# Kernel optimization log

Measured on AMD Instinct MI355X. Metric: run time of the kernel, lower is better.

The kernel has to match this reference:

```python
import jax, jax.numpy as jnp
import numpy as np
import math

N_EMBED = 1024
N_HEAD = 16
HS = N_EMBED // N_HEAD

def setup_inputs() -> dict:
    key = jax.random.key(0)
    ks = jax.random.split(key, 5)
    s = 1.0 / math.sqrt(N_EMBED)
    x = jax.random.normal(ks[0], (2, 2048, N_EMBED), dtype=jnp.float32)
    W_qkv = jax.random.uniform(ks[1], (N_EMBED, 3 * N_EMBED), dtype=jnp.float32, minval=-s, maxval=s)
    b_qkv = jax.random.uniform(ks[2], (3 * N_EMBED,), dtype=jnp.float32, minval=-s, maxval=s)
    W_out = jax.random.uniform(ks[3], (N_EMBED, N_EMBED), dtype=jnp.float32, minval=-s, maxval=s)
    b_out = jax.random.uniform(ks[4], (N_EMBED,), dtype=jnp.float32, minval=-s, maxval=s)
    return {"x": x, "W_qkv": W_qkv, "b_qkv": b_qkv, "W_out": W_out, "b_out": b_out}

def reference(x, W_qkv, b_qkv, W_out, b_out):
    bs, seq_len, dim = x.shape
    qkv = x @ W_qkv + b_qkv                      # [b, s, 3*d]
    q, k, v = jnp.split(qkv, 3, axis=-1)
    def heads(t):
        return t.reshape(bs, seq_len, N_HEAD, HS).transpose(0, 2, 1, 3)  # [b, h, s, hs]
    q, k, v = heads(q), heads(k), heads(v)
    scale = 1.0 / math.sqrt(HS)
    attn = jnp.einsum('bhqd,bhkd->bhqk', q, k) * scale  # [b, h, s, s]
    causal = jnp.tril(jnp.ones((seq_len, seq_len), dtype=bool))
    attn = jnp.where(causal, attn, -jnp.inf)
    attn = jax.nn.softmax(attn, axis=-1)
    o = jnp.einsum('bhqk,bhkd->bhqd', attn, v)   # [b, h, s, hs]
    o = o.transpose(0, 2, 1, 3).reshape(bs, seq_len, dim)
    return o @ W_out + b_out
```

## Files before the change

### kernel.cpp

```cpp
#include <hip/hip_runtime.h>
#include <hip/hip_bf16.h>
#include <stdint.h>

typedef __attribute__((ext_vector_type(4))) float f32x4;
typedef __attribute__((ext_vector_type(8))) short s16x8;
typedef __attribute__((ext_vector_type(4))) short s16x4;

#define B_   2
#define S_   2048
#define D_   1024
#define H_   16
#define HS_  64
#define TOK  (B_*S_)
#define BH_  (B_*H_)

__device__ __forceinline__ short f2bf(float f){
  union { float f; uint32_t u; } v; v.f = f;
  uint32_t u = v.u;
  u += 0x7fffu + ((u >> 16) & 1u);
  return (short)(u >> 16);
}

__device__ __forceinline__ uint32_t cvt_pk_bf16(float lo, float hi){
  uint32_t r;
  asm("v_cvt_pk_bf16_f32 %0, %1, %2" : "=v"(r) : "v"(lo), "v"(hi));
  return r;
}

__device__ __forceinline__ void gload_lds16(const void* g, void* l){
  __builtin_amdgcn_global_load_lds((const __attribute__((address_space(1))) void*)g,
                                   (__attribute__((address_space(3))) void*)l, 16, 0, 0);
}

__global__ void k_cvt(const float* __restrict__ src, short* __restrict__ dst, int n4){
  int i = blockIdx.x * blockDim.x + threadIdx.x;
  if (i < n4){
    float4 v = reinterpret_cast<const float4*>(src)[i];
    s16x4 o;
    o.x = f2bf(v.x); o.y = f2bf(v.y); o.z = f2bf(v.z); o.w = f2bf(v.w);
    reinterpret_cast<s16x4*>(dst)[i] = o;
  }
}

__global__ void k_tconv(const float* __restrict__ src, short* __restrict__ dst, int K, int N){
  __shared__ short tile[32][33];
  const int n0 = blockIdx.x * 32, k0 = blockIdx.y * 32;
  const int c = threadIdx.x & 31, r8 = threadIdx.x >> 5;
  #pragma unroll
  for (int j = 0; j < 4; j++){
    int k = r8 + j * 8;
    tile[c][k] = f2bf(src[(size_t)(k0 + k) * N + n0 + c]);
  }
  __syncthreads();
  #pragma unroll
  for (int j = 0; j < 4; j++){
    int nl = r8 + j * 8;
    dst[(size_t)(n0 + nl) * K + k0 + c] = tile[nl][c];
  }
}

template<int EPI>
__global__ __launch_bounds__(256, 2) void k_gemm(
    const short* __restrict__ A, const short* __restrict__ Bt,
    const float* __restrict__ bias, void* __restrict__ outp)
{
  __shared__ short Al[128 * 32];
  __shared__ short Bl[128 * 32];
  const int tid = threadIdx.x;
  const int lane = tid & 63, wave = tid >> 6;
  const int m0 = blockIdx.x * 128, n0 = blockIdx.y * 128;
  const int wm = (wave >> 1) * 64, wn = (wave & 1) * 64;
  const int c = lane & 15, g = lane >> 4;

  f32x4 acc[4][4];
  #pragma unroll
  for (int i = 0; i < 4; i++)
    #pragma unroll
    for (int j = 0; j < 4; j++) acc[i][j] = (f32x4){0.f, 0.f, 0.f, 0.f};

  const short* Asrc = A + (size_t)m0 * 1024;
  const short* Bsrc = Bt + (size_t)n0 * 1024;

  for (int kt = 0; kt < 1024; kt += 32){
    __syncthreads();
    #pragma unroll
    for (int j = 0; j < 2; j++){
      int gc = (wave * 2 + j) * 64 + lane;
      int row = gc >> 2, c8 = gc & 3;
      gload_lds16(Asrc + (size_t)row * 1024 + kt + c8 * 8, Al + (size_t)(wave * 2 + j) * 512);
      gload_lds16(Bsrc + (size_t)row * 1024 + kt + c8 * 8, Bl + (size_t)(wave * 2 + j) * 512);
    }
    __syncthreads();

    s16x8 af[4], bq[4];
    #pragma unroll
    for (int t = 0; t < 4; t++){
      af[t] = *(const s16x8*)&Al[(wm + t * 16 + c) * 32 + g * 8];
      bq[t] = *(const s16x8*)&Bl[(wn + t * 16 + c) * 32 + g * 8];
    }
    #pragma unroll
    for (int mt = 0; mt < 4; mt++)
      #pragma unroll
      for (int nt = 0; nt < 4; nt++)
        acc[mt][nt] = __builtin_amdgcn_mfma_f32_16x16x32_bf16(af[mt], bq[nt], acc[mt][nt], 0, 0, 0);
  }

  if (EPI == 0){
    short* Qb = (short*)outp;
    const size_t QSZ = (size_t)BH_ * S_ * HS_;
    #pragma unroll
    for (int mt = 0; mt < 4; mt++){
      #pragma unroll
      for (int nt = 0; nt < 4; nt++){
        int n = n0 + wn + nt * 16 + c;
        float bv = bias[n];
        int sel = n >> 10, hn = (n >> 6) & 15, d = n & 63;
        #pragma unroll
        for (int r = 0; r < 4; r++){
          int token = m0 + wm + mt * 16 + g * 4 + r;
          int b = token >> 11, s = token & 2047;
          float v = acc[mt][nt][r] + bv;
          Qb[(size_t)sel * QSZ + ((size_t)(b * H_ + hn) * S_ + s) * HS_ + d] = f2bf(v);
        }
      }
    }
  } else {
    float* O = (float*)outp;
    #pragma unroll
    for (int mt = 0; mt < 4; mt++){
      #pragma unroll
      for (int nt = 0; nt < 4; nt++){
        int n = n0 + wn + nt * 16 + c;
        float bv = bias[n];
        #pragma unroll
        for (int r = 0; r < 4; r++){
          int token = m0 + wm + mt * 16 + g * 4 + r;
          O[(size_t)token * 1024 + n] = acc[mt][nt][r] + bv;
        }
      }
    }
  }
}

__global__ void k_vtrans(const short* __restrict__ Vg, short* __restrict__ Vt){
  __shared__ short t[64 * 80];
  const int bh = blockIdx.y;
  const int s0 = blockIdx.x * 64;
  const int tid = threadIdx.x;
  const int r = tid >> 3, c8 = (tid & 7) * 8;
  #pragma unroll
  for (int p = 0; p < 2; p++){
    int ss = r + p * 32;
    s16x8 v = *(const s16x8*)&Vg[((size_t)bh * S_ + s0 + ss) * HS_ + c8];
    #pragma unroll
    for (int i = 0; i < 8; i++) t[(c8 + i) * 80 + ss] = v[i];
  }
  __syncthreads();
  #pragma unroll
  for (int p = 0; p < 2; p++){
    int d = r + p * 32;
    s16x8 v = *(const s16x8*)&t[d * 80 + c8];
    *(s16x8*)&Vt[((size_t)bh * HS_ + d) * S_ + s0 + c8] = v;
  }
}

__global__ __launch_bounds__(256, 3) void k_attn(
    const short* __restrict__ Qg, const short* __restrict__ Kg,
    const short* __restrict__ Vt, short* __restrict__ Og)
{
  __shared__ short Kl[2][64 * 64];
  __shared__ short Vl[2][64 * 64];
  __shared__ short Pl[4][32 * 64];

  const int tid = threadIdx.x, lane = tid & 63, wave = tid >> 6;
  const int c = lane & 15, g = lane >> 4;
  const int c7 = c & 7;

  const int p = blockIdx.x;
  const int qt = 15 - (p >> 5);
  const int bh = p & 31;
  const int q0 = qt * 128;
  const int q0w = q0 + wave * 32;
  const int nkt = 2 * qt + 2;
  const size_t basebh = (size_t)bh * S_ * HS_;
  const short* Kb  = Kg + basebh;
  const short* Vtb = Vt + (size_t)bh * HS_ * S_;

  s16x8 qb[2][2];
  #pragma unroll
  for (int rt = 0; rt < 2; rt++)
    #pragma unroll
    for (int h = 0; h < 2; h++)
      qb[rt][h] = *(const s16x8*)&Qg[basebh + (size_t)(q0w + rt * 16 + c) * HS_ + h * 32 + g * 8];

  f32x4 o_acc[2][4];
  #pragma unroll
  for (int rt = 0; rt < 2; rt++)
    #pragma unroll
    for (int nt = 0; nt < 4; nt++) o_acc[rt][nt] = (f32x4){0.f, 0.f, 0.f, 0.f};
  float m_[2] = {-3e38f, -3e38f}, l_[2] = {0.f, 0.f};

  short* Pw = &Pl[wave][0];
  const float SC = 0.125f * 1.44269504f;

  const int srow = tid >> 3;
  const int schk = tid & 7;
  const int swc  = ((schk ^ (srow & 7)) * 8);
  const int ldsoff0 = wave * 512;

  auto STAGE = [&](int buf, int kt){
    const int k0 = kt * 64;
    #pragma unroll
    for (int i = 0; i < 2; i++){
      gload_lds16(Kb + (size_t)(k0 + srow + 32 * i) * HS_ + swc, &Kl[buf][i * 2048 + ldsoff0]);
      gload_lds16(Vtb + (size_t)(srow + 32 * i) * S_ + k0 + swc, &Vl[buf][i * 2048 + ldsoff0]);
    }
  };

  auto COMPUTE = [&](int buf, int kt){
    const int k0 = kt * 64;
    const short* KB = &Kl[buf][0];
    const short* VB = &Vl[buf][0];

    s16x8 ka[4][2];
    #pragma unroll
    for (int kf = 0; kf < 4; kf++)
      #pragma unroll
      for (int h = 0; h < 2; h++)
        ka[kf][h] = *(const s16x8*)&KB[(kf * 16 + c) * 64 + ((h * 4 + g) ^ c7) * 8];

    #pragma unroll
    for (int rt = 0; rt < 2; rt++){
      const int qlo = q0w + rt * 16;
      if (k0 > qlo + 15) continue;

      f32x4 st[4];
      #pragma unroll
      for (int kf = 0; kf < 4; kf++){
        f32x4 a = (f32x4){0.f, 0.f, 0.f, 0.f};
        a = __builtin_amdgcn_mfma_f32_16x16x32_bf16(ka[kf][0], qb[rt][0], a, 0, 0, 0);
        a = __builtin_amdgcn_mfma_f32_16x16x32_bf16(ka[kf][1], qb[rt][1], a, 0, 0, 0);
        st[kf] = a;
      }

      const bool edge = (k0 + 63 > qlo);
      float sc[16];
      float tmax = -3e38f;
      #pragma unroll
      for (int kf = 0; kf < 4; kf++)
        #pragma unroll
        for (int r = 0; r < 4; r++){
          float v = st[kf][r] * SC;
          if (edge && (k0 + kf * 16 + g * 4 + r > qlo + c)) v = -3e38f;
          sc[kf * 4 + r] = v;
          tmax = fmaxf(tmax, v);
        }
      tmax = fmaxf(tmax, __shfl_xor(tmax, 16));
      tmax = fmaxf(tmax, __shfl_xor(tmax, 32));

      if (!__all(tmax <= m_[rt])){
        float mnew = fmaxf(m_[rt], tmax);
        float fe = exp2f(m_[rt] - mnew);
        m_[rt] = mnew;
        l_[rt] *= fe;
        float feq0 = __shfl(fe, g * 4 + 0), feq1 = __shfl(fe, g * 4 + 1);
        float feq2 = __shfl(fe, g * 4 + 2), feq3 = __shfl(fe, g * 4 + 3);
        #pragma unroll
        for (int nt = 0; nt < 4; nt++){
          f32x4 t = o_acc[rt][nt];
          t[0] *= feq0; t[1] *= feq1; t[2] *= feq2; t[3] *= feq3;
          o_acc[rt][nt] = t;
        }
      }

      float rs = 0.f;
      const int prow = rt * 16 + c;
      #pragma unroll
      for (int kf = 0; kf < 4; kf++){
        float p0 = exp2f(sc[kf * 4 + 0] - m_[rt]);
        float p1 = exp2f(sc[kf * 4 + 1] - m_[rt]);
        float p2 = exp2f(sc[kf * 4 + 2] - m_[rt]);
        float p3 = exp2f(sc[kf * 4 + 3] - m_[rt]);
        rs += (p0 + p1) + (p2 + p3);
        uint2 pk;
        pk.x = cvt_pk_bf16(p0, p1);
        pk.y = cvt_pk_bf16(p2, p3);
        *(uint2*)&Pw[prow * 64 + ((2 * kf + (g >> 1)) ^ c7) * 8 + (g & 1) * 4] = pk;
      }
      rs += __shfl_xor(rs, 16);
      rs += __shfl_xor(rs, 32);
      l_[rt] += rs;
    }

    s16x8 vb[4][2];
    #pragma unroll
    for (int nt = 0; nt < 4; nt++)
      #pragma unroll
      for (int ks = 0; ks < 2; ks++)
        vb[nt][ks] = *(const s16x8*)&VB[(nt * 16 + c) * 64 + ((ks * 4 + g) ^ c7) * 8];

    #pragma unroll
    for (int rt = 0; rt < 2; rt++){
      if (k0 > q0w + rt * 16 + 15) continue;
      #pragma unroll
      for (int ks = 0; ks < 2; ks++){
        s16x8 pa = *(const s16x8*)&Pw[(rt * 16 + c) * 64 + ((ks * 4 + g) ^ c7) * 8];
        #pragma unroll
        for (int nt = 0; nt < 4; nt++)
          o_acc[rt][nt] = __builtin_amdgcn_mfma_f32_16x16x32_bf16(pa, vb[nt][ks], o_acc[rt][nt], 0, 0, 0);
      }
    }
  };

  STAGE(0, 0);
  __syncthreads();
  int cur = 0;
  for (int t = 0; t < nkt; t++){
    if (t + 1 < nkt) STAGE(cur ^ 1, t + 1);
    COMPUTE(cur, t);
    __syncthreads();
    cur ^= 1;
  }

  const int h = bh & 15, b = bh >> 4;
  #pragma unroll
  for (int rt = 0; rt < 2; rt++){
    float linv = 1.0f / l_[rt];
    float lr0 = __shfl(linv, g * 4 + 0), lr1 = __shfl(linv, g * 4 + 1);
    float lr2 = __shfl(linv, g * 4 + 2), lr3 = __shfl(linv, g * 4 + 3);
    #pragma unroll
    for (int nt = 0; nt < 4; nt++){
      int q = q0w + rt * 16 + g * 4;
      size_t base = (size_t)(b * S_ + q) * D_ + h * HS_ + nt * 16 + c;
      Og[base]            = f2bf(o_acc[rt][nt][0] * lr0);
      Og[base + D_]       = f2bf(o_acc[rt][nt][1] * lr1);
      Og[base + 2 * D_]   = f2bf(o_acc[rt][nt][2] * lr2);
      Og[base + 3 * D_]   = f2bf(o_acc[rt][nt][3] * lr3);
    }
  }
}

extern "C" void kernel_launch(void* const* d_in, const int* in_sizes, int n_in,
                              void* d_out, int out_size, void* d_ws, size_t ws_size,
                              hipStream_t stream)
{
  const float* x    = (const float*)d_in[0];
  const float* Wqkv = (const float*)d_in[1];
  const float* bqkv = (const float*)d_in[2];
  const float* Wout = (const float*)d_in[3];
  const float* bout = (const float*)d_in[4];

  char* ws = (char*)d_ws;
  short* xb     = (short*)(ws);
  short* Wqkv_t = (short*)(ws + 8388608);
  short* Wout_t = (short*)(ws + 14680064);
  short* Qg     = (short*)(ws + 16777216);
  short* Kg     = Qg + 4194304;
  short* Vg     = Qg + 8388608;
  short* Vt     = (short*)(ws + 41943040);
  short* Otok   = xb;

  k_cvt<<<4096, 256, 0, stream>>>(x, xb, TOK * D_ / 4);
  k_tconv<<<dim3(96, 32), 256, 0, stream>>>(Wqkv, Wqkv_t, 1024, 3072);
  k_tconv<<<dim3(32, 32), 256, 0, stream>>>(Wout, Wout_t, 1024, 1024);
  k_gemm<0><<<dim3(32, 24), 256, 0, stream>>>(xb, Wqkv_t, bqkv, (void*)Qg);
  k_vtrans<<<dim3(32, 32), 256, 0, stream>>>(Vg, Vt);
  k_attn<<<dim3(512), 256, 0, stream>>>(Qg, Kg, Vt, Otok);
  k_gemm<1><<<dim3(32, 8), 256, 0, stream>>>(Otok, Wout_t, bout, d_out);
}
```

Before: 222.2 us.

## Split output GEMM into smaller tiles, rebalance attention tile order, fold scale into exp

The output projection gets its own kernel with 64x128 tiles, launching 512 blocks instead of 256 so more CUs are busy on the smaller GEMM. Attention blocks past the first 256 now take query tiles in ascending order, pairing heavy and light causal tiles across the two halves of the grid. The softmax scale is moved out of the score loop into an fma inside exp2 and into the rescale factor, saving one multiply per score. Smaller GEMM tiles lower per-block data reuse, and the max is now tracked on unscaled scores.

```diff
diff --git a/kernel.cpp b/kernel.cpp
--- a/kernel.cpp
+++ b/kernel.cpp
@@ -59,10 +59,9 @@
   }
 }
 
-template<int EPI>
-__global__ __launch_bounds__(256, 2) void k_gemm(
+__global__ __launch_bounds__(256, 2) void k_gemm_qkv(
     const short* __restrict__ A, const short* __restrict__ Bt,
-    const float* __restrict__ bias, void* __restrict__ outp)
+    const float* __restrict__ bias, short* __restrict__ Qb)
 {
   __shared__ short Al[128 * 32];
   __shared__ short Bl[128 * 32];
@@ -105,38 +104,85 @@
         acc[mt][nt] = __builtin_amdgcn_mfma_f32_16x16x32_bf16(af[mt], bq[nt], acc[mt][nt], 0, 0, 0);
   }
 
-  if (EPI == 0){
-    short* Qb = (short*)outp;
-    const size_t QSZ = (size_t)BH_ * S_ * HS_;
-    #pragma unroll
-    for (int mt = 0; mt < 4; mt++){
-      #pragma unroll
-      for (int nt = 0; nt < 4; nt++){
-        int n = n0 + wn + nt * 16 + c;
-        float bv = bias[n];
-        int sel = n >> 10, hn = (n >> 6) & 15, d = n & 63;
-        #pragma unroll
-        for (int r = 0; r < 4; r++){
-          int token = m0 + wm + mt * 16 + g * 4 + r;
-          int b = token >> 11, s = token & 2047;
-          float v = acc[mt][nt][r] + bv;
-          Qb[(size_t)sel * QSZ + ((size_t)(b * H_ + hn) * S_ + s) * HS_ + d] = f2bf(v);
-        }
-      }
-    }
-  } else {
-    float* O = (float*)outp;
-    #pragma unroll
-    for (int mt = 0; mt < 4; mt++){
-      #pragma unroll
-      for (int nt = 0; nt < 4; nt++){
-        int n = n0 + wn + nt * 16 + c;
-        float bv = bias[n];
-        #pragma unroll
-        for (int r = 0; r < 4; r++){
-          int token = m0 + wm + mt * 16 + g * 4 + r;
-          O[(size_t)token * 1024 + n] = acc[mt][nt][r] + bv;
-        }
+  const size_t QSZ = (size_t)BH_ * S_ * HS_;
+  #pragma unroll
+  for (int mt = 0; mt < 4; mt++){
+    #pragma unroll
+    for (int nt = 0; nt < 4; nt++){
+      int n = n0 + wn + nt * 16 + c;
+      float bv = bias[n];
+      int sel = n >> 10, hn = (n >> 6) & 15, d = n & 63;
+      #pragma unroll
+      for (int r = 0; r < 4; r++){
+        int token = m0 + wm + mt * 16 + g * 4 + r;
+        int b = token >> 11, s = token & 2047;
+        float v = acc[mt][nt][r] + bv;
+        Qb[(size_t)sel * QSZ + ((size_t)(b * H_ + hn) * S_ + s) * HS_ + d] = f2bf(v);
+      }
+    }
+  }
+}
+
+__global__ __launch_bounds__(256, 2) void k_gemm_o(
+    const short* __restrict__ A, const short* __restrict__ Bt,
+    const float* __restrict__ bias, float* __restrict__ O)
+{
+  __shared__ short Al[64 * 32];
+  __shared__ short Bl[128 * 32];
+  const int tid = threadIdx.x;
+  const int lane = tid & 63, wave = tid >> 6;
+  const int m0 = blockIdx.x * 64, n0 = blockIdx.y * 128;
+  const int wn = wave * 32;
+  const int c = lane & 15, g = lane >> 4;
+
+  f32x4 acc[4][2];
+  #pragma unroll
+  for (int i = 0; i < 4; i++)
+    #pragma unroll
+    for (int j = 0; j < 2; j++) acc[i][j] = (f32x4){0.f, 0.f, 0.f, 0.f};
+
+  const short* Asrc = A + (size_t)m0 * 1024;
+  const short* Bsrc = Bt + (size_t)n0 * 1024;
+
+  for (int kt = 0; kt < 1024; kt += 32){
+    __syncthreads();
+    {
+      int gc = wave * 64 + lane;
+      int row = gc >> 2, c8 = gc & 3;
+      gload_lds16(Asrc + (size_t)row * 1024 + kt + c8 * 8, Al + (size_t)wave * 512);
+    }
+    #pragma unroll
+    for (int j = 0; j < 2; j++){
+      int gc = (wave * 2 + j) * 64 + lane;
+      int row = gc >> 2, c8 = gc & 3;
+      gload_lds16(Bsrc + (size_t)row * 1024 + kt + c8 * 8, Bl + (size_t)(wave * 2 + j) * 512);
+    }
+    __syncthreads();
+
+    s16x8 af[4], bq[2];
+    #pragma unroll
+    for (int t = 0; t < 4; t++)
+      af[t] = *(const s16x8*)&Al[(t * 16 + c) * 32 + g * 8];
+    #pragma unroll
+    for (int n = 0; n < 2; n++)
+      bq[n] = *(const s16x8*)&Bl[(wn + n * 16 + c) * 32 + g * 8];
+    #pragma unroll
+    for (int mt = 0; mt < 4; mt++)
+      #pragma unroll
+      for (int n = 0; n < 2; n++)
+        acc[mt][n] = __builtin_amdgcn_mfma_f32_16x16x32_bf16(af[mt], bq[n], acc[mt][n], 0, 0, 0);
+  }
+
+  #pragma unroll
+  for (int mt = 0; mt < 4; mt++){
+    #pragma unroll
+    for (int n = 0; n < 2; n++){
+      int nn = n0 + wn + n * 16 + c;
+      float bv = bias[nn];
+      #pragma unroll
+      for (int r = 0; r < 4; r++){
+        int token = m0 + mt * 16 + g * 4 + r;
+        O[(size_t)token * 1024 + nn] = acc[mt][n][r] + bv;
       }
     }
   }
@@ -177,7 +223,7 @@
   const int c7 = c & 7;
 
   const int p = blockIdx.x;
-  const int qt = 15 - (p >> 5);
+  const int qt = (p < 256) ? (15 - (p >> 5)) : ((p - 256) >> 5);
   const int bh = p & 31;
   const int q0 = qt * 128;
   const int q0w = q0 + wave * 32;
@@ -250,7 +296,7 @@
       for (int kf = 0; kf < 4; kf++)
         #pragma unroll
         for (int r = 0; r < 4; r++){
-          float v = st[kf][r] * SC;
+          float v = st[kf][r];
           if (edge && (k0 + kf * 16 + g * 4 + r > qlo + c)) v = -3e38f;
           sc[kf * 4 + r] = v;
           tmax = fmaxf(tmax, v);
@@ -260,7 +306,7 @@
 
       if (!__all(tmax <= m_[rt])){
         float mnew = fmaxf(m_[rt], tmax);
-        float fe = exp2f(m_[rt] - mnew);
+        float fe = exp2f((m_[rt] - mnew) * SC);
         m_[rt] = mnew;
         l_[rt] *= fe;
         float feq0 = __shfl(fe, g * 4 + 0), feq1 = __shfl(fe, g * 4 + 1);
@@ -273,14 +319,15 @@
         }
       }
 
+      const float nmsc = -m_[rt] * SC;
       float rs = 0.f;
       const int prow = rt * 16 + c;
       #pragma unroll
       for (int kf = 0; kf < 4; kf++){
-        float p0 = exp2f(sc[kf * 4 + 0] - m_[rt]);
-        float p1 = exp2f(sc[kf * 4 + 1] - m_[rt]);
-        float p2 = exp2f(sc[kf * 4 + 2] - m_[rt]);
-        float p3 = exp2f(sc[kf * 4 + 3] - m_[rt]);
+        float p0 = exp2f(fmaf(sc[kf * 4 + 0], SC, nmsc));
+        float p1 = exp2f(fmaf(sc[kf * 4 + 1], SC, nmsc));
+        float p2 = exp2f(fmaf(sc[kf * 4 + 2], SC, nmsc));
+        float p3 = exp2f(fmaf(sc[kf * 4 + 3], SC, nmsc));
         rs += (p0 + p1) + (p2 + p3);
         uint2 pk;
         pk.x = cvt_pk_bf16(p0, p1);
@@ -363,8 +410,8 @@
   k_cvt<<<4096, 256, 0, stream>>>(x, xb, TOK * D_ / 4);
   k_tconv<<<dim3(96, 32), 256, 0, stream>>>(Wqkv, Wqkv_t, 1024, 3072);
   k_tconv<<<dim3(32, 32), 256, 0, stream>>>(Wout, Wout_t, 1024, 1024);
-  k_gemm<0><<<dim3(32, 24), 256, 0, stream>>>(xb, Wqkv_t, bqkv, (void*)Qg);
+  k_gemm_qkv<<<dim3(32, 24), 256, 0, stream>>>(xb, Wqkv_t, bqkv, Qg);
   k_vtrans<<<dim3(32, 32), 256, 0, stream>>>(Vg, Vt);
   k_attn<<<dim3(512), 256, 0, stream>>>(Qg, Kg, Vt, Otok);
-  k_gemm<1><<<dim3(32, 8), 256, 0, stream>>>(Otok, Wout_t, bout, d_out);
-}
+  k_gemm_o<<<dim3(64, 8), 256, 0, stream>>>(Otok, Wout_t, bout, (float*)d_out);
+}
```

New measurement: 221.9 us. No clear change (-0.2%).
